# Performance work log

Measured on AMD Instinct MI355X. Metric: run time of the kernel, lower is better.

Reference implementation:

```python
import jax, jax.numpy as jnp
import numpy as np

J, N, C = 24, 131072, 16
GS = (128, 128, 128)
MAT = ((0, 1), (0, 2), (1, 2))  # matMode
VEC = (2, 1, 0)                 # vecMode


def _bilinear(plane, xy):
    # plane: (C, H, W); xy: (N, 2) in [-1, 1]; align_corners=True grid_sample
    Cc, H, W = plane.shape
    x = (xy[:, 0] + 1.0) * 0.5 * (W - 1)
    y = (xy[:, 1] + 1.0) * 0.5 * (H - 1)
    x0 = jnp.clip(jnp.floor(x), 0, W - 1)
    y0 = jnp.clip(jnp.floor(y), 0, H - 1)
    x1 = jnp.clip(x0 + 1, 0, W - 1)
    y1 = jnp.clip(y0 + 1, 0, H - 1)
    wx = x - x0
    wy = y - y0
    x0i, x1i, y0i, y1i = (a.astype(jnp.int32) for a in (x0, x1, y0, y1))
    v00 = plane[:, y0i, x0i]  # (C, N)
    v01 = plane[:, y0i, x1i]
    v10 = plane[:, y1i, x0i]
    v11 = plane[:, y1i, x1i]
    top = v00 * (1.0 - wx) + v01 * wx
    bot = v10 * (1.0 - wx) + v11 * wx
    return top * (1.0 - wy) + bot * wy  # (C, N)


def _linear1d(line, z):
    # line: (C, L); z: (N,) in [-1, 1]; 1D version (grid x coord is 0, width 1)
    Cc, L = line.shape
    y = (z + 1.0) * 0.5 * (L - 1)
    y0 = jnp.clip(jnp.floor(y), 0, L - 1)
    y1 = jnp.clip(y0 + 1, 0, L - 1)
    wy = y - y0
    v0 = line[:, y0.astype(jnp.int32)]  # (C, N)
    v1 = line[:, y1.astype(jnp.int32)]
    return v0 * (1.0 - wy) + v1 * wy


def setup_inputs() -> dict:
    key = jax.random.key(0)
    ks = jax.random.split(key, 7)
    xyz = jax.random.uniform(ks[0], (J, N, 3), jnp.float32) * 2.0 - 1.0
    scale = 1.0
    def p_init(k, shape):
        return -(scale * 0.5) + 0.1 + scale * jax.random.normal(k, shape, jnp.float32)
    inp = {"xyz_sampled": xyz}
    for i in range(3):
        m0, m1 = MAT[i]
        inp[f"plane{i}"] = p_init(ks[1 + i], (J, C, GS[m1], GS[m0]))
        inp[f"line{i}"] = p_init(ks[4 + i], (J, C, GS[VEC[i]]))
    return inp


def reference(xyz_sampled, plane0, plane1, plane2, line0, line1, line2):
    planes = (plane0, plane1, plane2)
    lines = (line0, line1, line2)
    feat = jnp.zeros(xyz_sampled.shape[:2], xyz_sampled.dtype)  # (J, N)
    for i in range(3):
        xy = jnp.stack([xyz_sampled[..., MAT[i][0]], xyz_sampled[..., MAT[i][1]]], axis=-1)  # (J,N,2)
        p = jax.vmap(_bilinear)(planes[i], xy)                 # (J, C, N)
        l = jax.vmap(_linear1d)(lines[i], xyz_sampled[..., VEC[i]])  # (J, C, N)
        feat = feat + jnp.sum(p * l, axis=1)
    return jax.nn.relu(feat)
```

## Files before the change

kernel.cpp:

```cpp
#include <hip/hip_runtime.h>
#include <hip/hip_fp16.h>
#include <stdint.h>

#define JB 24
#define NP 131072
#define CH 16
#define G  128

#define PLANE_H2 (JB*G*G*CH)
#define LINE_H2  (JB*G*CH)

typedef _Float16 h2_t __attribute__((ext_vector_type(2)));
typedef unsigned int u32x4 __attribute__((ext_vector_type(4)));

__device__ __forceinline__ float fdot2(uint32_t a, h2_t w, float c) {
#if __has_builtin(__builtin_amdgcn_fdot2)
    return __builtin_amdgcn_fdot2(__builtin_bit_cast(h2_t, a), w, c, false);
#else
    __half2 ha = __builtin_bit_cast(__half2, a);
    float2 fa = __half22float2(ha);
    h2_t wv = w;
    return c + fa.x * (float)wv[0] + fa.y * (float)wv[1];
#endif
}

__global__ __launch_bounds__(256)
void pack_planes_kernel(const float* __restrict__ p0,
                        const float* __restrict__ p1,
                        const float* __restrict__ p2,
                        __half2* __restrict__ wsp) {
    __shared__ float lds[CH * (G + 1)];
    int b = blockIdx.x;
    int y = b & (G - 1);
    int j = (b >> 7) % JB;
    int p = b / (G * JB);
    const float* src = (p == 0 ? p0 : (p == 1 ? p1 : p2))
                       + ((size_t)j * CH) * (G * G) + (size_t)y * G;
    __half2* dst = wsp + ((size_t)(p * JB + j) * G + y) * (G * CH);
    int tid = threadIdx.x;
    for (int idx = tid; idx < G * CH; idx += 256) {
        int c = idx >> 7;
        int x = idx & (G - 1);
        lds[c * (G + 1) + x] = src[(size_t)c * G * G + x];
    }
    __syncthreads();
    for (int idx = tid; idx < G * CH; idx += 256) {
        int x = idx >> 4;
        int c = idx & 15;
        int x1 = (x < G - 1) ? x + 1 : x;
        float a = lds[c * (G + 1) + x];
        float bvv = lds[c * (G + 1) + x1];
        dst[idx] = __floats2half2_rn(a, bvv);
    }
}

__global__ __launch_bounds__(256)
void pack_lines_kernel(const float* __restrict__ l0,
                       const float* __restrict__ l1,
                       const float* __restrict__ l2,
                       __half2* __restrict__ wsl) {
    int gid = blockIdx.x * 256 + threadIdx.x;
    if (gid >= 3 * LINE_H2) return;
    int p = gid / LINE_H2;
    int r = gid - p * LINE_H2;
    int j = r >> 11;
    int z = (r >> 4) & (G - 1);
    int c = r & 15;
    int z1 = (z < G - 1) ? z + 1 : z;
    const float* src = (p == 0 ? l0 : (p == 1 ? l1 : l2));
    float a = src[((size_t)j * CH + c) * G + z];
    float bvv = src[((size_t)j * CH + c) * G + z1];
    wsl[gid] = __floats2half2_rn(a, bvv);
}

__global__ __launch_bounds__(1024)
void tensorf_lds1k_kernel(const float* __restrict__ xyz,
                          const uint32_t* __restrict__ wp,
                          const uint32_t* __restrict__ wl,
                          float* __restrict__ out) {
    const int NWG = (JB * NP) / 1024;
    int bid = blockIdx.x;
    int wg = (bid & 7) * (NWG >> 3) + (bid >> 3);
    int tid = threadIdx.x;
    int ptblk = wg << 10;
    int j = ptblk >> 17;

    __shared__ uint32_t slines[3 * 2048];
    {
        u32x4* dst4 = (u32x4*)slines;
        for (int idx = tid; idx < 1536; idx += 1024) {
            int i = idx >> 9;
            int r = idx & 511;
            dst4[idx] = ((const u32x4*)(wl + (((size_t)i * JB + j) << 11)))[r];
        }
    }
    __syncthreads();

    int l4 = tid & 3;
    int slot = tid >> 2;

    const int M0[3] = {0, 0, 1};
    const int M1[3] = {1, 2, 2};
    const int VZ[3] = {2, 1, 0};

    #pragma unroll
    for (int p = 0; p < 4; ++p) {
        int pt = ptblk + (p << 8) + slot;

        float cx = xyz[(size_t)pt * 3 + 0];
        float cy = xyz[(size_t)pt * 3 + 1];
        float cz = xyz[(size_t)pt * 3 + 2];
        const float co[3] = {cx, cy, cz};

        float4 acc = {0.f, 0.f, 0.f, 0.f};
        #pragma unroll
        for (int i = 0; i < 3; ++i) {
            float fx = (co[M0[i]] + 1.f) * 63.5f;
            float fy = (co[M1[i]] + 1.f) * 63.5f;
            float fz = (co[VZ[i]] + 1.f) * 63.5f;
            float f0x = floorf(fx);
            float f0y = floorf(fy);
            float f0z = floorf(fz);
            int x0 = (int)f0x, y0 = (int)f0y, z0 = (int)f0z;
            float wx = fx - f0x, wy = fy - f0y, wz = fz - f0z;

            h2_t wxh = {(_Float16)(1.f - wx), (_Float16)wx};
            h2_t wzh = {(_Float16)(1.f - wz), (_Float16)wz};

            int pb = ((i * JB + j) << 18) + (((y0 << 7) + x0) << 4) + (l4 << 2);
            u32x4 A = *(const u32x4*)(wp + pb);
            u32x4 B = *(const u32x4*)(wp + pb + (G << 4));
            u32x4 C = *(const u32x4*)(slines + (i << 11) + (z0 << 4) + (l4 << 2));

            float t0 = fdot2(A.x, wxh, 0.f);
            float t1 = fdot2(A.y, wxh, 0.f);
            float t2 = fdot2(A.z, wxh, 0.f);
            float t3 = fdot2(A.w, wxh, 0.f);
            float b0 = fdot2(B.x, wxh, 0.f);
            float b1 = fdot2(B.y, wxh, 0.f);
            float b2 = fdot2(B.z, wxh, 0.f);
            float b3 = fdot2(B.w, wxh, 0.f);
            float v0 = fdot2(C.x, wzh, 0.f);
            float v1 = fdot2(C.y, wzh, 0.f);
            float v2 = fdot2(C.z, wzh, 0.f);
            float v3 = fdot2(C.w, wzh, 0.f);
            float q0 = t0 + (b0 - t0) * wy;
            float q1 = t1 + (b1 - t1) * wy;
            float q2 = t2 + (b2 - t2) * wy;
            float q3 = t3 + (b3 - t3) * wy;
            acc.x = fmaf(q0, v0, acc.x);
            acc.y = fmaf(q1, v1, acc.y);
            acc.z = fmaf(q2, v2, acc.z);
            acc.w = fmaf(q3, v3, acc.w);
        }
        float s = (acc.x + acc.y) + (acc.z + acc.w);
        s += __shfl_xor(s, 1);
        s += __shfl_xor(s, 2);
        if (l4 == 0) out[pt] = fmaxf(s, 0.f);
    }
}

__global__ __launch_bounds__(256)
void tensorf_direct_kernel(const float* __restrict__ xyz,
                           const float* __restrict__ p0,
                           const float* __restrict__ p1,
                           const float* __restrict__ p2,
                           const float* __restrict__ l0,
                           const float* __restrict__ l1,
                           const float* __restrict__ l2,
                           float* __restrict__ out) {
    int gid = blockIdx.x * 256 + threadIdx.x;
    if (gid >= JB * NP) return;
    int j = gid >> 17;
    float cx = xyz[(size_t)gid * 3 + 0];
    float cy = xyz[(size_t)gid * 3 + 1];
    float cz = xyz[(size_t)gid * 3 + 2];
    const float co[3] = {cx, cy, cz};
    const int M0[3] = {0, 0, 1};
    const int M1[3] = {1, 2, 2};
    const int VZ[3] = {2, 1, 0};
    const float* PP[3] = {p0, p1, p2};
    const float* LL[3] = {l0, l1, l2};

    float acc = 0.f;
    #pragma unroll
    for (int i = 0; i < 3; ++i) {
        float fx = (co[M0[i]] + 1.f) * 63.5f;
        float fy = (co[M1[i]] + 1.f) * 63.5f;
        float fz = (co[VZ[i]] + 1.f) * 63.5f;
        float f0x = fminf(fmaxf(floorf(fx), 0.f), 127.f);
        float f0y = fminf(fmaxf(floorf(fy), 0.f), 127.f);
        float f0z = fminf(fmaxf(floorf(fz), 0.f), 127.f);
        int x0 = (int)f0x, y0 = (int)f0y, z0 = (int)f0z;
        int x1 = min(x0 + 1, G - 1);
        int y1 = min(y0 + 1, G - 1);
        int z1 = min(z0 + 1, G - 1);
        float wx = fx - f0x, wy = fy - f0y, wz = fz - f0z;

        const float* p = PP[i] + (size_t)j * CH * G * G;
        const float* l = LL[i] + (size_t)j * CH * G;
        for (int c = 0; c < CH; ++c) {
            const float* pc = p + (size_t)c * G * G;
            float v00 = pc[(size_t)y0 * G + x0];
            float v01 = pc[(size_t)y0 * G + x1];
            float v10 = pc[(size_t)y1 * G + x0];
            float v11 = pc[(size_t)y1 * G + x1];
            float lc0 = l[(size_t)c * G + z0];
            float lc1 = l[(size_t)c * G + z1];
            float top = v00 + (v01 - v00) * wx;
            float bot = v10 + (v11 - v10) * wx;
            float pv  = top + (bot - top) * wy;
            float lv  = lc0 + (lc1 - lc0) * wz;
            acc += pv * lv;
        }
    }
    out[gid] = fmaxf(acc, 0.f);
}

extern "C" void kernel_launch(void* const* d_in, const int* in_sizes, int n_in,
                              void* d_out, int out_size, void* d_ws, size_t ws_size,
                              hipStream_t stream) {
    const float* xyz = (const float*)d_in[0];
    const float* p0  = (const float*)d_in[1];
    const float* l0  = (const float*)d_in[2];
    const float* p1  = (const float*)d_in[3];
    const float* l1  = (const float*)d_in[4];
    const float* p2  = (const float*)d_in[5];
    const float* l2  = (const float*)d_in[6];
    float* out = (float*)d_out;

    const size_t need = ((size_t)3 * PLANE_H2 + (size_t)3 * LINE_H2) * sizeof(__half2);
    const int npts = JB * NP;

    if (ws_size >= need) {
        __half2* wsp = (__half2*)d_ws;
        __half2* wsl = wsp + (size_t)3 * PLANE_H2;
        pack_planes_kernel<<<3 * JB * G, 256, 0, stream>>>(p0, p1, p2, wsp);
        pack_lines_kernel<<<(3 * LINE_H2 + 255) / 256, 256, 0, stream>>>(l0, l1, l2, wsl);
        const int nblocks = npts / 1024;
        tensorf_lds1k_kernel<<<nblocks, 1024, 0, stream>>>(
            xyz, (const uint32_t*)wsp, (const uint32_t*)wsl, out);
    } else {
        tensorf_direct_kernel<<<(npts + 255) / 256, 256, 0, stream>>>(xyz, p0, p1, p2, l0, l1, l2, out);
    }
}
```

Baseline: 121.2 us.

## Bucket-sort sample points by spatial Morton key before gathering planes

Adds a per-batch counting sort (histogram, scan, scatter) that groups points into 8x8x8-cell Morton-ordered buckets, then runs the fp16 gather kernel over the sorted points and writes each result back to its original index. This is meant to improve cache locality of the random plane gathers, which dominate memory traffic. It costs three extra passes over the points, a memset, global atomics and a scattered output write.

```diff
diff --git a/kernel.cpp b/kernel.cpp
--- a/kernel.cpp
+++ b/kernel.cpp
@@ -6,9 +6,12 @@
 #define NP 131072
 #define CH 16
 #define G  128
+#define NPTS (JB*NP)
 
 #define PLANE_H2 (JB*G*G*CH)
 #define LINE_H2  (JB*G*CH)
+#define NBUCK_J  4096
+#define NBUCK    (JB*NBUCK_J)
 
 typedef _Float16 h2_t __attribute__((ext_vector_type(2)));
 typedef unsigned int u32x4 __attribute__((ext_vector_type(4)));
@@ -22,6 +25,18 @@
     h2_t wv = w;
     return c + fa.x * (float)wv[0] + fa.y * (float)wv[1];
 #endif
+}
+
+__device__ __forceinline__ uint32_t spread3_4(uint32_t v) {
+    return (v & 1u) | ((v & 2u) << 2) | ((v & 4u) << 4) | ((v & 8u) << 6);
+}
+
+__device__ __forceinline__ uint32_t bucket_key(float cx, float cy, float cz) {
+    int x0 = (int)floorf((cx + 1.f) * 63.5f);
+    int y0 = (int)floorf((cy + 1.f) * 63.5f);
+    int z0 = (int)floorf((cz + 1.f) * 63.5f);
+    uint32_t bx = (uint32_t)x0 >> 3, by = (uint32_t)y0 >> 3, bz = (uint32_t)z0 >> 3;
+    return spread3_4(bx) | (spread3_4(by) << 1) | (spread3_4(bz) << 2);
 }
 
 __global__ __launch_bounds__(256)
@@ -73,12 +88,63 @@
     wsl[gid] = __floats2half2_rn(a, bvv);
 }
 
+__global__ __launch_bounds__(256)
+void hist_kernel(const float* __restrict__ xyz, uint32_t* __restrict__ cnt) {
+    int pt = blockIdx.x * 256 + threadIdx.x;
+    if (pt >= NPTS) return;
+    int j = pt >> 17;
+    float cx = xyz[(size_t)pt * 3 + 0];
+    float cy = xyz[(size_t)pt * 3 + 1];
+    float cz = xyz[(size_t)pt * 3 + 2];
+    uint32_t key = (uint32_t)j * NBUCK_J + bucket_key(cx, cy, cz);
+    atomicAdd(&cnt[key], 1u);
+}
+
 __global__ __launch_bounds__(1024)
-void tensorf_lds1k_kernel(const float* __restrict__ xyz,
-                          const uint32_t* __restrict__ wp,
-                          const uint32_t* __restrict__ wl,
-                          float* __restrict__ out) {
-    const int NWG = (JB * NP) / 1024;
+void scan_kernel(uint32_t* __restrict__ cnt) {
+    __shared__ uint32_t part[1024];
+    int j = blockIdx.x;
+    int t = threadIdx.x;
+    u32x4* c = (u32x4*)(cnt + (size_t)j * NBUCK_J);
+    u32x4 v = c[t];
+    uint32_t s = v.x + v.y + v.z + v.w;
+    part[t] = s;
+    __syncthreads();
+    for (int off = 1; off < 1024; off <<= 1) {
+        uint32_t q = (t >= off) ? part[t - off] : 0u;
+        __syncthreads();
+        part[t] += q;
+        __syncthreads();
+    }
+    uint32_t excl = part[t] - s + (uint32_t)j * NP;
+    u32x4 o;
+    o.x = excl;
+    o.y = excl + v.x;
+    o.z = o.y + v.y;
+    o.w = o.z + v.z;
+    c[t] = o;
+}
+
+__global__ __launch_bounds__(256)
+void scatter_kernel(const float* __restrict__ xyz, uint32_t* __restrict__ off,
+                    float4* __restrict__ pdata) {
+    int pt = blockIdx.x * 256 + threadIdx.x;
+    if (pt >= NPTS) return;
+    int j = pt >> 17;
+    float cx = xyz[(size_t)pt * 3 + 0];
+    float cy = xyz[(size_t)pt * 3 + 1];
+    float cz = xyz[(size_t)pt * 3 + 2];
+    uint32_t key = (uint32_t)j * NBUCK_J + bucket_key(cx, cy, cz);
+    uint32_t pos = atomicAdd(&off[key], 1u);
+    pdata[pos] = make_float4(cx, cy, cz, __int_as_float(pt));
+}
+
+__global__ __launch_bounds__(1024)
+void tensorf_sorted_kernel(const float4* __restrict__ pdata,
+                           const uint32_t* __restrict__ wp,
+                           const uint32_t* __restrict__ wl,
+                           float* __restrict__ out) {
+    const int NWG = NPTS / 1024;
     int bid = blockIdx.x;
     int wg = (bid & 7) * (NWG >> 3) + (bid >> 3);
     int tid = threadIdx.x;
@@ -105,12 +171,9 @@
 
     #pragma unroll
     for (int p = 0; p < 4; ++p) {
-        int pt = ptblk + (p << 8) + slot;
-
-        float cx = xyz[(size_t)pt * 3 + 0];
-        float cy = xyz[(size_t)pt * 3 + 1];
-        float cz = xyz[(size_t)pt * 3 + 2];
-        const float co[3] = {cx, cy, cz};
+        int g = ptblk + (p << 8) + slot;
+        float4 pd = pdata[g];
+        const float co[3] = {pd.x, pd.y, pd.z};
 
         float4 acc = {0.f, 0.f, 0.f, 0.f};
         #pragma unroll
@@ -156,6 +219,80 @@
         float s = (acc.x + acc.y) + (acc.z + acc.w);
         s += __shfl_xor(s, 1);
         s += __shfl_xor(s, 2);
+        if (l4 == 0) out[__float_as_int(pd.w)] = fmaxf(s, 0.f);
+    }
+}
+
+__global__ __launch_bounds__(1024)
+void tensorf_lds1k_kernel(const float* __restrict__ xyz,
+                          const uint32_t* __restrict__ wp,
+                          const uint32_t* __restrict__ wl,
+                          float* __restrict__ out) {
+    const int NWG = NPTS / 1024;
+    int bid = blockIdx.x;
+    int wg = (bid & 7) * (NWG >> 3) + (bid >> 3);
+    int tid = threadIdx.x;
+    int ptblk = wg << 10;
+    int j = ptblk >> 17;
+
+    __shared__ uint32_t slines[3 * 2048];
+    {
+        u32x4* dst4 = (u32x4*)slines;
+        for (int idx = tid; idx < 1536; idx += 1024) {
+            int i = idx >> 9;
+            int r = idx & 511;
+            dst4[idx] = ((const u32x4*)(wl + (((size_t)i * JB + j) << 11)))[r];
+        }
+    }
+    __syncthreads();
+
+    int l4 = tid & 3;
+    int slot = tid >> 2;
+    const int M0[3] = {0, 0, 1};
+    const int M1[3] = {1, 2, 2};
+    const int VZ[3] = {2, 1, 0};
+
+    #pragma unroll
+    for (int p = 0; p < 4; ++p) {
+        int pt = ptblk + (p << 8) + slot;
+        float cx = xyz[(size_t)pt * 3 + 0];
+        float cy = xyz[(size_t)pt * 3 + 1];
+        float cz = xyz[(size_t)pt * 3 + 2];
+        const float co[3] = {cx, cy, cz};
+
+        float4 acc = {0.f, 0.f, 0.f, 0.f};
+        #pragma unroll
+        for (int i = 0; i < 3; ++i) {
+            float fx = (co[M0[i]] + 1.f) * 63.5f;
+            float fy = (co[M1[i]] + 1.f) * 63.5f;
+            float fz = (co[VZ[i]] + 1.f) * 63.5f;
+            float f0x = floorf(fx);
+            float f0y = floorf(fy);
+            float f0z = floorf(fz);
+            int x0 = (int)f0x, y0 = (int)f0y, z0 = (int)f0z;
+            float wx = fx - f0x, wy = fy - f0y, wz = fz - f0z;
+            h2_t wxh = {(_Float16)(1.f - wx), (_Float16)wx};
+            h2_t wzh = {(_Float16)(1.f - wz), (_Float16)wz};
+            int pb = ((i * JB + j) << 18) + (((y0 << 7) + x0) << 4) + (l4 << 2);
+            u32x4 A = *(const u32x4*)(wp + pb);
+            u32x4 B = *(const u32x4*)(wp + pb + (G << 4));
+            u32x4 C = *(const u32x4*)(slines + (i << 11) + (z0 << 4) + (l4 << 2));
+            float t0 = fdot2(A.x, wxh, 0.f), t1 = fdot2(A.y, wxh, 0.f);
+            float t2 = fdot2(A.z, wxh, 0.f), t3 = fdot2(A.w, wxh, 0.f);
+            float b0 = fdot2(B.x, wxh, 0.f), b1 = fdot2(B.y, wxh, 0.f);
+            float b2 = fdot2(B.z, wxh, 0.f), b3 = fdot2(B.w, wxh, 0.f);
+            float v0 = fdot2(C.x, wzh, 0.f), v1 = fdot2(C.y, wzh, 0.f);
+            float v2 = fdot2(C.z, wzh, 0.f), v3 = fdot2(C.w, wzh, 0.f);
+            float q0 = t0 + (b0 - t0) * wy, q1 = t1 + (b1 - t1) * wy;
+            float q2 = t2 + (b2 - t2) * wy, q3 = t3 + (b3 - t3) * wy;
+            acc.x = fmaf(q0, v0, acc.x);
+            acc.y = fmaf(q1, v1, acc.y);
+            acc.z = fmaf(q2, v2, acc.z);
+            acc.w = fmaf(q3, v3, acc.w);
+        }
+        float s = (acc.x + acc.y) + (acc.z + acc.w);
+        s += __shfl_xor(s, 1);
+        s += __shfl_xor(s, 2);
         if (l4 == 0) out[pt] = fmaxf(s, 0.f);
     }
 }
@@ -170,7 +307,7 @@
                            const float* __restrict__ l2,
                            float* __restrict__ out) {
     int gid = blockIdx.x * 256 + threadIdx.x;
-    if (gid >= JB * NP) return;
+    if (gid >= NPTS) return;
     int j = gid >> 17;
     float cx = xyz[(size_t)gid * 3 + 0];
     float cy = xyz[(size_t)gid * 3 + 1];
@@ -229,18 +366,38 @@
     const float* l2  = (const float*)d_in[6];
     float* out = (float*)d_out;
 
-    const size_t need = ((size_t)3 * PLANE_H2 + (size_t)3 * LINE_H2) * sizeof(__half2);
-    const int npts = JB * NP;
-
-    if (ws_size >= need) {
-        __half2* wsp = (__half2*)d_ws;
-        __half2* wsl = wsp + (size_t)3 * PLANE_H2;
+    const size_t off_wsp  = 0;
+    const size_t off_wsl  = off_wsp + (size_t)3 * PLANE_H2;
+    const size_t off_cnt  = off_wsl + (size_t)3 * LINE_H2;
+    const size_t off_pd   = off_cnt + NBUCK;
+    const size_t total_sort = off_pd + (size_t)NPTS * 4;
+    const size_t need_sort = total_sort * 4;
+    const size_t need_r9   = (off_cnt) * 4;
+
+    uint32_t* wsu = (uint32_t*)d_ws;
+
+    if (ws_size >= need_sort) {
+        __half2* wsp = (__half2*)(wsu + off_wsp);
+        __half2* wsl = (__half2*)(wsu + off_wsl);
+        uint32_t* cnt = wsu + off_cnt;
+        float4* pdata = (float4*)(wsu + off_pd);
+
         pack_planes_kernel<<<3 * JB * G, 256, 0, stream>>>(p0, p1, p2, wsp);
         pack_lines_kernel<<<(3 * LINE_H2 + 255) / 256, 256, 0, stream>>>(l0, l1, l2, wsl);
-        const int nblocks = npts / 1024;
-        tensorf_lds1k_kernel<<<nblocks, 1024, 0, stream>>>(
+        hipMemsetAsync(cnt, 0, NBUCK * sizeof(uint32_t), stream);
+        hist_kernel<<<NPTS / 256, 256, 0, stream>>>(xyz, cnt);
+        scan_kernel<<<JB, 1024, 0, stream>>>(cnt);
+        scatter_kernel<<<NPTS / 256, 256, 0, stream>>>(xyz, cnt, pdata);
+        tensorf_sorted_kernel<<<NPTS / 1024, 1024, 0, stream>>>(
+            pdata, (const uint32_t*)wsp, (const uint32_t*)wsl, out);
+    } else if (ws_size >= need_r9) {
+        __half2* wsp = (__half2*)(wsu + off_wsp);
+        __half2* wsl = (__half2*)(wsu + off_wsl);
+        pack_planes_kernel<<<3 * JB * G, 256, 0, stream>>>(p0, p1, p2, wsp);
+        pack_lines_kernel<<<(3 * LINE_H2 + 255) / 256, 256, 0, stream>>>(l0, l1, l2, wsl);
+        tensorf_lds1k_kernel<<<NPTS / 1024, 1024, 0, stream>>>(
             xyz, (const uint32_t*)wsp, (const uint32_t*)wsl, out);
     } else {
-        tensorf_direct_kernel<<<(npts + 255) / 256, 256, 0, stream>>>(xyz, p0, p1, p2, l0, l1, l2, out);
-    }
-}
+        tensorf_direct_kernel<<<(NPTS + 255) / 256, 256, 0, stream>>>(xyz, p0, p1, p2, l0, l1, l2, out);
+    }
+}
```

After: 353.9 us. 2.92x slower.
